# Kernel optimization log

Measured on AMD Instinct MI355X. Metric: run time of the kernel, lower is better.

The kernel has to match this reference:

```python
import jax, jax.numpy as jnp
import numpy as np

EMA = 0.999
EPS = 1e-8


def setup_inputs() -> dict:
    key = jax.random.key(0)
    k1, k2, k3 = jax.random.split(key, 3)
    B, z_dim, H, W = 16, 64, 32, 32
    M = 4096
    N = B * H * W
    return {
        "z": jax.random.normal(k1, (B, z_dim, H, W), dtype=jnp.float32),
        "e": jax.random.normal(k2, (M, z_dim), dtype=jnp.float32),
        "belong": jax.random.uniform(k3, (N, M), dtype=jnp.float32),
        "log_sigma": jnp.zeros((1,), dtype=jnp.float32),
        "max_distance": jnp.ones((1, M), dtype=jnp.float32),
        "distance_p": 2,
    }


def reference(z, e, belong, log_sigma, max_distance, distance_p):
    B, z_dim, H, W = z.shape
    # [B, z_dim, H, W] -> [N, z_dim], N = B*H*W
    zf = jnp.transpose(z, (0, 2, 3, 1)).reshape(-1, z_dim)
    # pairwise L2 distance via GEMM expansion: ||z||^2 + ||e||^2 - 2 z.e
    d2 = (jnp.sum(zf * zf, axis=1, keepdims=True)
          + jnp.sum(e * e, axis=1)[None, :]
          - 2.0 * (zf @ e.T))                      # [N, M]
    distance = jnp.sqrt(jnp.maximum(d2, 0.0))
    # EMA update of per-code max distance (buffer, no grad in original)
    batch_max = jnp.max(belong * distance, axis=0, keepdims=True)  # [1, M]
    new_max = EMA * max_distance + (1.0 - EMA) * batch_max
    new_max = jax.lax.stop_gradient(jnp.clip(new_max, EPS, None))
    p = float(distance_p)
    distance = jnp.where(distance < new_max,
                         distance ** (2.0 / p),
                         distance ** (2.0 * p))
    alpha = -1.0 / (2.0 * jnp.exp(log_sigma) ** 2)  # shape (1,)
    lse = jax.scipy.special.logsumexp(alpha * distance, axis=0)  # [M]
    loss = -jnp.mean(lse) + z_dim * log_sigma  # shape (1,), as in torch
    return loss
```

## Files before the change

### kernel.cpp

```cpp
#include <hip/hip_runtime.h>
#include <hip/hip_bf16.h>

#define ZD   64
#define MM   4096
#define NN   16384
#define HWSZ 1024
#define BB   16

typedef __bf16 bf16x8 __attribute__((ext_vector_type(8)));
typedef float  f32x4  __attribute__((ext_vector_type(4)));

#define EMA_C 0.999f
#define EPS_C 1e-8f

__global__ __launch_bounds__(256) void k_prep(const float* __restrict__ z,
                                              const float* __restrict__ e,
                                              __hip_bfloat16* __restrict__ zf,
                                              __hip_bfloat16* __restrict__ ebf,
                                              float* __restrict__ zn2,
                                              float* __restrict__ en2,
                                              unsigned* __restrict__ bmax,
                                              unsigned* __restrict__ dmin,
                                              float* __restrict__ sume) {
    __shared__ float tile[64][65];
    __shared__ float part[4][64];
    int blk = blockIdx.x;
    int tid = threadIdx.x;
    if (blk < 256) {
        int b   = blk >> 4;
        int hw0 = (blk & 15) * 64;
        int tx = tid & 63, ty = tid >> 6;
        const float* zp = z + (size_t)b * (ZD * HWSZ);
#pragma unroll
        for (int kk = 0; kk < 16; kk++) {
            int k = kk * 4 + ty;
            tile[k][tx] = zp[(size_t)k * HWSZ + hw0 + tx];
        }
        __syncthreads();
#pragma unroll
        for (int i = 0; i < 16; i++) {
            int li = tid + i * 256;
            int ln = li >> 6, lk = li & 63;
            int n = b * HWSZ + hw0 + ln;
            zf[(size_t)n * ZD + lk] = __float2bfloat16(tile[lk][ln]);
        }
        float s = 0.f;
#pragma unroll
        for (int kk = 0; kk < 16; kk++) {
            float q = __bfloat162float(__float2bfloat16(tile[ty * 1 + kk * 4][tx]));
            s += q * q;
        }
        part[ty][tx] = s;
        __syncthreads();
        if (tid < 64) {
            float t = part[0][tid] + part[1][tid] + part[2][tid] + part[3][tid];
            zn2[b * HWSZ + hw0 + tid] = t;
        }
    } else {
        int eb  = blk - 256;
        int gid = eb * 256 + tid;
        if (gid < MM) {
            bmax[gid] = 0u;
            dmin[gid] = 0x7f800000u;
            sume[gid] = 0.f;
        }
        int wave = tid >> 6, lane = tid & 63;
        int row = eb * 4 + wave;
        if (row < MM) {
            float v = e[row * ZD + lane];
            __hip_bfloat16 b16 = __float2bfloat16(v);
            ebf[row * ZD + lane] = b16;
            float q = __bfloat162float(b16);
            float s = q * q;
            for (int off = 32; off; off >>= 1) s += __shfl_xor(s, off);
            if (lane == 0) en2[row] = s;
        }
    }
}

__global__ __launch_bounds__(256) void k_pass1(const __hip_bfloat16* __restrict__ zf,
                                               const __hip_bfloat16* __restrict__ ebf,
                                               const float* __restrict__ zn2,
                                               const float* __restrict__ en2,
                                               const float* __restrict__ belong,
                                               unsigned* __restrict__ bmax,
                                               unsigned* __restrict__ dmin) {
    int tid = threadIdx.x;
    int wave = tid >> 6, lane = tid & 63;
    int l16 = lane & 15, lq = lane >> 4;
    int wm = wave & 1, wn = wave >> 1;
    int m0 = blockIdx.x * 64 + wm * 32;
    int n0 = blockIdx.y * 128 + wn * 64;

    const bf16x8* ebv = reinterpret_cast<const bf16x8*>(ebf);
    const bf16x8* zfv = reinterpret_cast<const bf16x8*>(zf);

    bf16x8 Af[2][2], Bf[4][2];
#pragma unroll
    for (int im = 0; im < 2; im++)
#pragma unroll
        for (int h = 0; h < 2; h++)
            Af[im][h] = ebv[(size_t)(m0 + im * 16 + l16) * 8 + h * 4 + lq];
#pragma unroll
    for (int jn = 0; jn < 4; jn++)
#pragma unroll
        for (int h = 0; h < 2; h++)
            Bf[jn][h] = zfv[(size_t)(n0 + jn * 16 + l16) * 8 + h * 4 + lq];

    f32x4 bl[2][4];
#pragma unroll
    for (int im = 0; im < 2; im++)
#pragma unroll
        for (int jn = 0; jn < 4; jn++) {
            const f32x4* bp = reinterpret_cast<const f32x4*>(
                belong + (size_t)(n0 + jn * 16 + l16) * MM + (m0 + im * 16 + lq * 4));
            bl[im][jn] = __builtin_nontemporal_load(bp);
        }

    f32x4 acc[2][4];
#pragma unroll
    for (int im = 0; im < 2; im++)
#pragma unroll
        for (int jn = 0; jn < 4; jn++) {
            acc[im][jn] = (f32x4){0.f, 0.f, 0.f, 0.f};
            acc[im][jn] = __builtin_amdgcn_mfma_f32_16x16x32_bf16(Af[im][0], Bf[jn][0], acc[im][jn], 0, 0, 0);
            acc[im][jn] = __builtin_amdgcn_mfma_f32_16x16x32_bf16(Af[im][1], Bf[jn][1], acc[im][jn], 0, 0, 0);
        }

    f32x4 en2v[2];
#pragma unroll
    for (int im = 0; im < 2; im++)
        en2v[im] = *reinterpret_cast<const f32x4*>(en2 + m0 + im * 16 + lq * 4);
    float zn2v[4];
#pragma unroll
    for (int jn = 0; jn < 4; jn++)
        zn2v[jn] = zn2[n0 + jn * 16 + l16];

    float vmax[2][4], vmin[2][4];
#pragma unroll
    for (int im = 0; im < 2; im++)
#pragma unroll
        for (int r = 0; r < 4; r++) { vmax[im][r] = 0.f; vmin[im][r] = 3.4e38f; }

#pragma unroll
    for (int im = 0; im < 2; im++)
#pragma unroll
        for (int jn = 0; jn < 4; jn++)
#pragma unroll
            for (int r = 0; r < 4; r++) {
                float d2 = en2v[im][r] + zn2v[jn] - 2.f * acc[im][jn][r];
                float d = sqrtf(fmaxf(d2, 0.f));
                vmax[im][r] = fmaxf(vmax[im][r], bl[im][jn][r] * d);
                vmin[im][r] = fminf(vmin[im][r], d);
            }

#pragma unroll
    for (int off = 1; off < 16; off <<= 1)
#pragma unroll
        for (int im = 0; im < 2; im++)
#pragma unroll
            for (int r = 0; r < 4; r++) {
                vmax[im][r] = fmaxf(vmax[im][r], __shfl_xor(vmax[im][r], off));
                vmin[im][r] = fminf(vmin[im][r], __shfl_xor(vmin[im][r], off));
            }

    __shared__ unsigned smax[64], smin[64];
    if (tid < 64) { smax[tid] = 0u; smin[tid] = 0x7f800000u; }
    __syncthreads();
    if (l16 == 0) {
#pragma unroll
        for (int im = 0; im < 2; im++)
#pragma unroll
            for (int r = 0; r < 4; r++) {
                int ml = wm * 32 + im * 16 + lq * 4 + r;
                atomicMax(&smax[ml], __float_as_uint(vmax[im][r]));
                atomicMin(&smin[ml], __float_as_uint(vmin[im][r]));
            }
    }
    __syncthreads();
    if (tid < 64) {
        atomicMax(&bmax[blockIdx.x * 64 + tid], smax[tid]);
        atomicMin(&dmin[blockIdx.x * 64 + tid], smin[tid]);
    }
}

__global__ __launch_bounds__(256) void k_pass2(const __hip_bfloat16* __restrict__ zf,
                                               const __hip_bfloat16* __restrict__ ebf,
                                               const float* __restrict__ zn2,
                                               const float* __restrict__ en2,
                                               const unsigned* __restrict__ bmax,
                                               const unsigned* __restrict__ dmin,
                                               const float* __restrict__ max_distance,
                                               const float* __restrict__ log_sigma,
                                               const int* __restrict__ pp,
                                               float* __restrict__ refs,
                                               float* __restrict__ sume) {
    __shared__ float snm2[128], sref[128], ssum[128];
    int tid = threadIdx.x;
    int wave = tid >> 6, lane = tid & 63;
    int l16 = lane & 15, lq = lane >> 4;
    int wn = wave >> 1, wm = wave & 1;
    int n0 = blockIdx.x * 64 + wn * 32;
    int m0 = blockIdx.y * 128 + wm * 64;

    int p = pp[0];
    float alpha = -0.5f * __expf(-2.f * log_sigma[0]);

    if (tid < 128) {
        int m = blockIdx.y * 128 + tid;
        float bm = __uint_as_float(bmax[m]);
        float dm = __uint_as_float(dmin[m]);
        float nm = fmaxf(EMA_C * max_distance[m] + (1.f - EMA_C) * bm, EPS_C);
        float tlow;
        if (p == 2) {
            float d4  = (dm * dm) * (dm * dm);
            float nm4 = (nm * nm) * (nm * nm);
            tlow = (dm < nm) ? fminf(dm, nm4) : d4;
        } else {
            float e1 = 2.f / (float)p, e2 = 2.f * (float)p;
            tlow = (dm < nm) ? fminf(powf(dm, e1), powf(nm, e2)) : powf(dm, e2);
        }
        float rf = alpha * tlow;
        snm2[tid] = nm * nm;
        sref[tid] = rf;
        ssum[tid] = 0.f;
        if (blockIdx.x == 0) refs[m] = rf;
    }
    __syncthreads();

    const bf16x8* zfv = reinterpret_cast<const bf16x8*>(zf);
    const bf16x8* ebv = reinterpret_cast<const bf16x8*>(ebf);

    bf16x8 Af[2][2], Bf[4][2];
#pragma unroll
    for (int i = 0; i < 2; i++)
#pragma unroll
        for (int h = 0; h < 2; h++)
            Af[i][h] = zfv[(size_t)(n0 + i * 16 + l16) * 8 + h * 4 + lq];
#pragma unroll
    for (int j = 0; j < 4; j++)
#pragma unroll
        for (int h = 0; h < 2; h++)
            Bf[j][h] = ebv[(size_t)(m0 + j * 16 + l16) * 8 + h * 4 + lq];

    f32x4 acc[2][4];
#pragma unroll
    for (int i = 0; i < 2; i++)
#pragma unroll
        for (int j = 0; j < 4; j++) {
            acc[i][j] = (f32x4){0.f, 0.f, 0.f, 0.f};
            acc[i][j] = __builtin_amdgcn_mfma_f32_16x16x32_bf16(Af[i][0], Bf[j][0], acc[i][j], 0, 0, 0);
            acc[i][j] = __builtin_amdgcn_mfma_f32_16x16x32_bf16(Af[i][1], Bf[j][1], acc[i][j], 0, 0, 0);
        }

    f32x4 zn2v[2];
#pragma unroll
    for (int i = 0; i < 2; i++)
        zn2v[i] = *reinterpret_cast<const f32x4*>(zn2 + n0 + i * 16 + lq * 4);

    bool p2 = (p == 2);
    float pe = (float)p, pi = 1.f / (float)p;

#pragma unroll
    for (int j = 0; j < 4; j++) {
        float en2v = en2[m0 + j * 16 + l16];
        float nm2v = snm2[wm * 64 + j * 16 + l16];
        float rfv  = sref[wm * 64 + j * 16 + l16];
        float csum = 0.f;
#pragma unroll
        for (int i = 0; i < 2; i++)
#pragma unroll
            for (int r = 0; r < 4; r++) {
                float d2c = fmaxf(zn2v[i][r] + en2v - 2.f * acc[i][j][r], 0.f);
                float t;
                if (p2) t = (d2c < nm2v) ? sqrtf(d2c) : d2c * d2c;
                else    t = powf(d2c, (d2c < nm2v) ? pi : pe);
                csum += __expf(fmaf(alpha, t, -rfv));
            }
        csum += __shfl_xor(csum, 16);
        csum += __shfl_xor(csum, 32);
        if (lane < 16) atomicAdd(&ssum[wm * 64 + j * 16 + lane], csum);
    }
    __syncthreads();
    if (tid < 128) atomicAdd(&sume[blockIdx.y * 128 + tid], ssum[tid]);
}

__global__ __launch_bounds__(256) void k_final(const float* __restrict__ refs,
                                               const float* __restrict__ sume,
                                               const float* __restrict__ log_sigma,
                                               float* __restrict__ out) {
    __shared__ float red[4];
    int tid = threadIdx.x;
    float a = 0.f;
    for (int m = tid; m < MM; m += 256)
        a += refs[m] + logf(fmaxf(sume[m], 1e-30f));
    for (int off = 32; off; off >>= 1) a += __shfl_xor(a, off);
    int wave = tid >> 6, lane = tid & 63;
    if (lane == 0) red[wave] = a;
    __syncthreads();
    if (tid == 0) {
        float t = red[0] + red[1] + red[2] + red[3];
        out[0] = -t / (float)MM + (float)ZD * log_sigma[0];
    }
}

extern "C" void kernel_launch(void* const* d_in, const int* in_sizes, int n_in,
                              void* d_out, int out_size, void* d_ws, size_t ws_size,
                              hipStream_t stream) {
    const float* z            = (const float*)d_in[0];
    const float* e            = (const float*)d_in[1];
    const float* belong       = (const float*)d_in[2];
    const float* log_sigma    = (const float*)d_in[3];
    const float* max_distance = (const float*)d_in[4];
    const int*   pp           = (const int*)d_in[5];
    float* out = (float*)d_out;

    char* ws = (char*)d_ws;
    __hip_bfloat16* zf  = (__hip_bfloat16*)(ws + 0);
    __hip_bfloat16* ebf = (__hip_bfloat16*)(ws + 2097152);
    float*    zn2  = (float*)(ws + 2621440);
    float*    en2  = (float*)(ws + 2686976);
    unsigned* bmax = (unsigned*)(ws + 2703360);
    unsigned* dmin = (unsigned*)(ws + 2719744);
    float*    refs = (float*)(ws + 2736128);
    float*    sume = (float*)(ws + 2752512);

    k_prep<<<1280, 256, 0, stream>>>(z, e, zf, ebf, zn2, en2, bmax, dmin, sume);
    k_pass1<<<dim3(MM / 64, NN / 128), 256, 0, stream>>>(zf, ebf, zn2, en2, belong, bmax, dmin);
    k_pass2<<<dim3(NN / 64, MM / 128), 256, 0, stream>>>(zf, ebf, zn2, en2, bmax, dmin,
                                                         max_distance, log_sigma, pp, refs, sume);
    k_final<<<1, 256, 0, stream>>>(refs, sume, log_sigma, out);
}
```

Before: 484.4 us.

## Track squared distances in pass1, write per-block partials, skip sqrt in pass2

Pass1 now works on squared distances, using bel*bel*d2 for the max since belong is nonnegative, so the per-element sqrt is dropped. Its global atomics are replaced by per-row-block partial max/min arrays, which pass2 reduces at block start before taking the sqrt. Pass2 also skips the sqrt branch unless some lane in the wave falls below the threshold. The costs are larger workspace traffic and a 128-way redundant partial reduction in every pass2 block. The squared form also relies on belong being nonnegative.

```diff
diff --git a/kernel.cpp b/kernel.cpp
--- a/kernel.cpp
+++ b/kernel.cpp
@@ -1,11 +1,12 @@
 #include <hip/hip_runtime.h>
 #include <hip/hip_bf16.h>
 
-#define ZD   64
-#define MM   4096
-#define NN   16384
-#define HWSZ 1024
-#define BB   16
+#define ZD    64
+#define MM    4096
+#define NN    16384
+#define HWSZ  1024
+#define BB    16
+#define NPART 128
 
 typedef __bf16 bf16x8 __attribute__((ext_vector_type(8)));
 typedef float  f32x4  __attribute__((ext_vector_type(4)));
@@ -19,8 +20,6 @@
                                               __hip_bfloat16* __restrict__ ebf,
                                               float* __restrict__ zn2,
                                               float* __restrict__ en2,
-                                              unsigned* __restrict__ bmax,
-                                              unsigned* __restrict__ dmin,
                                               float* __restrict__ sume) {
     __shared__ float tile[64][65];
     __shared__ float part[4][64];
@@ -47,7 +46,7 @@
         float s = 0.f;
 #pragma unroll
         for (int kk = 0; kk < 16; kk++) {
-            float q = __bfloat162float(__float2bfloat16(tile[ty * 1 + kk * 4][tx]));
+            float q = __bfloat162float(__float2bfloat16(tile[ty + kk * 4][tx]));
             s += q * q;
         }
         part[ty][tx] = s;
@@ -59,11 +58,7 @@
     } else {
         int eb  = blk - 256;
         int gid = eb * 256 + tid;
-        if (gid < MM) {
-            bmax[gid] = 0u;
-            dmin[gid] = 0x7f800000u;
-            sume[gid] = 0.f;
-        }
+        if (gid < MM) sume[gid] = 0.f;
         int wave = tid >> 6, lane = tid & 63;
         int row = eb * 4 + wave;
         if (row < MM) {
@@ -83,8 +78,8 @@
                                                const float* __restrict__ zn2,
                                                const float* __restrict__ en2,
                                                const float* __restrict__ belong,
-                                               unsigned* __restrict__ bmax,
-                                               unsigned* __restrict__ dmin) {
+                                               float* __restrict__ pmax,
+                                               float* __restrict__ pmin) {
     int tid = threadIdx.x;
     int wave = tid >> 6, lane = tid & 63;
     int l16 = lane & 15, lq = lane >> 4;
@@ -148,10 +143,10 @@
         for (int jn = 0; jn < 4; jn++)
 #pragma unroll
             for (int r = 0; r < 4; r++) {
-                float d2 = en2v[im][r] + zn2v[jn] - 2.f * acc[im][jn][r];
-                float d = sqrtf(fmaxf(d2, 0.f));
-                vmax[im][r] = fmaxf(vmax[im][r], bl[im][jn][r] * d);
-                vmin[im][r] = fminf(vmin[im][r], d);
+                float d2  = fmaf(-2.f, acc[im][jn][r], en2v[im][r] + zn2v[jn]);
+                float bel = bl[im][jn][r];
+                vmax[im][r] = fmaxf(vmax[im][r], bel * bel * d2);
+                vmin[im][r] = fminf(vmin[im][r], d2);
             }
 
 #pragma unroll
@@ -164,8 +159,9 @@
                 vmin[im][r] = fminf(vmin[im][r], __shfl_xor(vmin[im][r], off));
             }
 
-    __shared__ unsigned smax[64], smin[64];
-    if (tid < 64) { smax[tid] = 0u; smin[tid] = 0x7f800000u; }
+    __shared__ unsigned smax[64];
+    __shared__ float    smin2[2][64];
+    if (tid < 64) smax[tid] = 0u;
     __syncthreads();
     if (l16 == 0) {
 #pragma unroll
@@ -173,14 +169,15 @@
 #pragma unroll
             for (int r = 0; r < 4; r++) {
                 int ml = wm * 32 + im * 16 + lq * 4 + r;
-                atomicMax(&smax[ml], __float_as_uint(vmax[im][r]));
-                atomicMin(&smin[ml], __float_as_uint(vmin[im][r]));
+                atomicMax(&smax[ml], __float_as_uint(fmaxf(vmax[im][r], 0.f)));
+                smin2[wn][ml] = vmin[im][r];
             }
     }
     __syncthreads();
     if (tid < 64) {
-        atomicMax(&bmax[blockIdx.x * 64 + tid], smax[tid]);
-        atomicMin(&dmin[blockIdx.x * 64 + tid], smin[tid]);
+        int m = blockIdx.x * 64 + tid;
+        pmax[(size_t)blockIdx.y * MM + m] = __uint_as_float(smax[tid]);
+        pmin[(size_t)blockIdx.y * MM + m] = fminf(smin2[0][tid], smin2[1][tid]);
     }
 }
 
@@ -188,28 +185,38 @@
                                                const __hip_bfloat16* __restrict__ ebf,
                                                const float* __restrict__ zn2,
                                                const float* __restrict__ en2,
-                                               const unsigned* __restrict__ bmax,
-                                               const unsigned* __restrict__ dmin,
+                                               const float* __restrict__ pmax,
+                                               const float* __restrict__ pmin,
                                                const float* __restrict__ max_distance,
                                                const float* __restrict__ log_sigma,
                                                const int* __restrict__ pp,
                                                float* __restrict__ refs,
                                                float* __restrict__ sume) {
+    __shared__ float sred[256];
     __shared__ float snm2[128], sref[128], ssum[128];
     int tid = threadIdx.x;
-    int wave = tid >> 6, lane = tid & 63;
-    int l16 = lane & 15, lq = lane >> 4;
-    int wn = wave >> 1, wm = wave & 1;
-    int n0 = blockIdx.x * 64 + wn * 32;
-    int m0 = blockIdx.y * 128 + wm * 64;
 
     int p = pp[0];
     float alpha = -0.5f * __expf(-2.f * log_sigma[0]);
 
+    {
+        int half = tid >> 7;
+        int col  = tid & 127;
+        int m    = blockIdx.y * 128 + col;
+        const float* base = (half ? pmin : pmax) + m;
+        float a0 = half ? 3.4e38f : 0.f;
+#pragma unroll 8
+        for (int yp = 0; yp < NPART; yp++) {
+            float v = base[(size_t)yp * MM];
+            a0 = half ? fminf(a0, v) : fmaxf(a0, v);
+        }
+        sred[tid] = a0;
+    }
+    __syncthreads();
     if (tid < 128) {
         int m = blockIdx.y * 128 + tid;
-        float bm = __uint_as_float(bmax[m]);
-        float dm = __uint_as_float(dmin[m]);
+        float bm = sqrtf(fmaxf(sred[tid], 0.f));
+        float dm = sqrtf(fmaxf(sred[tid + 128], 0.f));
         float nm = fmaxf(EMA_C * max_distance[m] + (1.f - EMA_C) * bm, EPS_C);
         float tlow;
         if (p == 2) {
@@ -228,6 +235,12 @@
     }
     __syncthreads();
 
+    int wave = tid >> 6, lane = tid & 63;
+    int l16 = lane & 15, lq = lane >> 4;
+    int wn = wave >> 1, wm = wave & 1;
+    int n0 = blockIdx.x * 64 + wn * 32;
+    int m0 = blockIdx.y * 128 + wm * 64;
+
     const bf16x8* zfv = reinterpret_cast<const bf16x8*>(zf);
     const bf16x8* ebv = reinterpret_cast<const bf16x8*>(ebf);
 
@@ -273,8 +286,13 @@
             for (int r = 0; r < 4; r++) {
                 float d2c = fmaxf(zn2v[i][r] + en2v - 2.f * acc[i][j][r], 0.f);
                 float t;
-                if (p2) t = (d2c < nm2v) ? sqrtf(d2c) : d2c * d2c;
-                else    t = powf(d2c, (d2c < nm2v) ? pi : pe);
+                if (p2) {
+                    t = d2c * d2c;
+                    if (__any(d2c < nm2v))
+                        t = (d2c < nm2v) ? sqrtf(d2c) : t;
+                } else {
+                    t = powf(d2c, (d2c < nm2v) ? pi : pe);
+                }
                 csum += __expf(fmaf(alpha, t, -rfv));
             }
         csum += __shfl_xor(csum, 16);
@@ -318,16 +336,16 @@
     char* ws = (char*)d_ws;
     __hip_bfloat16* zf  = (__hip_bfloat16*)(ws + 0);
     __hip_bfloat16* ebf = (__hip_bfloat16*)(ws + 2097152);
-    float*    zn2  = (float*)(ws + 2621440);
-    float*    en2  = (float*)(ws + 2686976);
-    unsigned* bmax = (unsigned*)(ws + 2703360);
-    unsigned* dmin = (unsigned*)(ws + 2719744);
-    float*    refs = (float*)(ws + 2736128);
-    float*    sume = (float*)(ws + 2752512);
-
-    k_prep<<<1280, 256, 0, stream>>>(z, e, zf, ebf, zn2, en2, bmax, dmin, sume);
-    k_pass1<<<dim3(MM / 64, NN / 128), 256, 0, stream>>>(zf, ebf, zn2, en2, belong, bmax, dmin);
-    k_pass2<<<dim3(NN / 64, MM / 128), 256, 0, stream>>>(zf, ebf, zn2, en2, bmax, dmin,
+    float* zn2  = (float*)(ws + 2621440);
+    float* en2  = (float*)(ws + 2686976);
+    float* pmax = (float*)(ws + 2703360);
+    float* pmin = (float*)(ws + 4800512);
+    float* refs = (float*)(ws + 6897664);
+    float* sume = (float*)(ws + 6914048);
+
+    k_prep<<<1280, 256, 0, stream>>>(z, e, zf, ebf, zn2, en2, sume);
+    k_pass1<<<dim3(MM / 64, NN / 128), 256, 0, stream>>>(zf, ebf, zn2, en2, belong, pmax, pmin);
+    k_pass2<<<dim3(NN / 64, MM / 128), 256, 0, stream>>>(zf, ebf, zn2, en2, pmax, pmin,
                                                          max_distance, log_sigma, pp, refs, sume);
     k_final<<<1, 256, 0, stream>>>(refs, sume, log_sigma, out);
 }
```

After: 561.3 us. 15.9% more time.
